# Optimization experiments

Hardware: AMD Instinct MI355X
Metric: run time of the kernel (lower is better)

Reference implementation:

```python
import jax, jax.numpy as jnp
import numpy as np

C, H, W = 21, 384, 384
THETA_ALPHA, THETA_BETA, THETA_GAMMA = 160.0, 3.0, 3.0
NUM_ITER = 5
SP_RADIUS = 6   # ~2*theta_gamma truncation for the spatial Gaussian filter
BI_RADIUS = 2   # local window stand-in for the permutohedral bilateral filter
CLIQUE_IDS = (5, 37, 81, 150, 230)  # deterministic stand-in for random.sample(range(1,256),5)


def _shift(x, dy, dx):
    # zero-padded shift: out[..., y, x] = x[..., y-dy, x-dx]
    h, w = x.shape[-2], x.shape[-1]
    py = (max(dy, 0), max(-dy, 0))
    px = (max(dx, 0), max(-dx, 0))
    xp = jnp.pad(x, [(0, 0)] * (x.ndim - 2) + [py, px])
    return xp[..., py[1]:py[1] + h, px[1]:px[1] + w]


def _gauss_blur(x, theta, radius):
    # unnormalized separable spatial Gaussian (high_dim_filter, bilateral=False)
    offs = np.arange(-radius, radius + 1)
    k = np.exp(-(offs.astype(np.float32) ** 2) / (2.0 * theta * theta))
    y = sum(float(k[i]) * _shift(x, int(o), 0) for i, o in enumerate(offs))
    return sum(float(k[i]) * _shift(y, 0, int(o)) for i, o in enumerate(offs))


def _bilateral(x, rgb, ta, tb, radius):
    # unnormalized local bilateral filter (high_dim_filter, bilateral=True)
    out = jnp.zeros_like(x)
    for dy in range(-radius, radius + 1):
        for dx in range(-radius, radius + 1):
            sw = float(np.exp(-(dy * dy + dx * dx) / (2.0 * ta * ta)))
            cdiff = rgb - _shift(rgb, dy, dx)  # (3,h,w)
            cw = jnp.exp(-jnp.sum(cdiff * cdiff, axis=0) / (2.0 * tb * tb))
            out = out + sw * cw * _shift(x, dy, dx)
    return out


def setup_inputs() -> dict:
    key = jax.random.key(0)
    k1, k2, k3 = jax.random.split(key, 3)
    # offset unaries away from 0 so first_term = prod/q stays finite
    unaries = jax.random.uniform(k1, (1, H, W, C), dtype=jnp.float32) + 0.5
    rgb = jax.random.uniform(k2, (1, H, W, 3), dtype=jnp.float32) * 255.0
    superpixels = jax.random.randint(k3, (1, H, W), 0, 256, dtype=jnp.int32)
    return {
        "unaries": unaries,
        "rgb": rgb,
        "superpixels": superpixels,
        "spatial_ker_weights": jnp.eye(C, dtype=jnp.float32),
        "bilateral_ker_weights": jnp.eye(C, dtype=jnp.float32),
        "compatibility_matrix": -jnp.eye(C, dtype=jnp.float32),
        "superpixel_low_weights": jnp.ones((C,), dtype=jnp.float32),
        "superpixel_high_weight": jnp.ones((1,), dtype=jnp.float32),
    }


def reference(unaries, rgb, superpixels, spatial_ker_weights, bilateral_ker_weights,
              compatibility_matrix, superpixel_low_weights, superpixel_high_weight):
    c, h, w = C, H, W
    u = jnp.transpose(unaries[0], (2, 0, 1))        # (c,h,w)
    img = jnp.transpose(rgb[0], (2, 0, 1))          # (3,h,w)
    sp_map = jnp.transpose(superpixels[0])          # (w,h) == (h,w) since square

    ones = jnp.ones((c, h, w), dtype=u.dtype)
    spatial_norm = _gauss_blur(ones, THETA_GAMMA, SP_RADIUS)
    bilateral_norm = _bilateral(ones, img, THETA_ALPHA, THETA_BETA, BI_RADIUS)

    # clique ids are distinct, so masks are disjoint; msum in {0,1}
    msum = jnp.zeros((h, w), dtype=u.dtype)
    for sp_idx in CLIQUE_IDS:
        msum = msum + (sp_map == sp_idx).astype(u.dtype)
    n_cliques = float(len(CLIQUE_IDS))

    q = u
    for _ in range(NUM_ITER):
        sm = jax.nn.softmax(q, axis=0)
        spatial_out = _gauss_blur(sm, THETA_GAMMA, SP_RADIUS) / spatial_norm
        bilateral_out = _bilateral(sm, img, THETA_ALPHA, THETA_BETA, BI_RADIUS) / bilateral_norm

        # prod_tensor = sum_k [ mask_k*q + (1-mask_k) ]  (disjoint masks => closed form)
        prod_tensor = msum[None] * q + (n_cliques - msum)[None]
        first_term = prod_tensor / q
        sp_update = (superpixel_low_weights[:, None, None] * first_term
                     + superpixel_high_weight[0] * (1.0 - first_term))

        mp = (spatial_ker_weights @ spatial_out.reshape(c, -1)
              + bilateral_ker_weights @ bilateral_out.reshape(c, -1))
        pairwise = (compatibility_matrix @ mp).reshape(c, h, w)
        q = u - pairwise + sp_update

    return jnp.transpose(q[None], (0, 2, 3, 1))  # (1,h,w,c)
```

## Files before the change

kernel.cpp:

```cpp
#include <hip/hip_runtime.h>
#include <hip/hip_bf16.h>

static constexpr int C  = 21;
static constexpr int H  = 384;
static constexpr int W  = 384;
static constexpr int HW = H * W;
static constexpr float NCLIQ = 5.0f;

typedef unsigned short u16;
typedef unsigned int   u32;

#define GKDEF constexpr float gk[13] = { \
    0.13533528f, 0.24935222f, 0.41111229f, 0.60653066f, 0.80073740f, \
    0.94595947f, 1.00000000f, 0.94595947f, 0.80073740f, 0.60653066f, \
    0.41111229f, 0.24935222f, 0.13533528f }

__device__ __forceinline__ float bfu2f(u16 u) {
    return __uint_as_float(((u32)u) << 16);
}
__device__ __forceinline__ u16 f2bfu(float f) {
    unsigned x = __float_as_uint(f);
    return (u16)((x + 0x7FFF + ((x >> 16) & 1)) >> 16);
}

__global__ __launch_bounds__(256)
void k_prep(const float* __restrict__ un, const float* __restrict__ rgb,
            const int* __restrict__ sp,
            const float* __restrict__ Wsp, const float* __restrict__ Wbi,
            const float* __restrict__ Cm,
            float* __restrict__ q, float* __restrict__ unp,
            u16* __restrict__ wtab, float* __restrict__ msum,
            float* __restrict__ inv_sp, float* __restrict__ inv_bn,
            float* __restrict__ M1, float* __restrict__ M2,
            int* __restrict__ mflag,
            u16* __restrict__ t1, u16* __restrict__ t2) {
    GKDEF;
    __shared__ float sM1[C * C], sM2[C * C];
    __shared__ float Aun[256 * C];
    __shared__ int seq;
    if (threadIdx.x == 0) seq = 1;
    bool bad = false;
    for (int i = threadIdx.x; i < C * C; i += 256) {
        int c = i / C, k = i - c * C;
        float a1 = 0.f, a2 = 0.f;
        for (int j = 0; j < C; j++) {
            float cm = Cm[c * C + j];
            a1 += cm * Wsp[j * C + k];
            a2 += cm * Wbi[j * C + k];
        }
        sM1[i] = a1;
        sM2[i] = a2;
        if (__float_as_uint(a1) != __float_as_uint(a2)) bad = true;
        if (blockIdx.x == 0) { M1[i] = a1; M2[i] = a2; }
    }

    int bid = blockIdx.x;
    int chunk = (bid & 7) * 72 + (bid >> 3);
    int p0 = chunk * 256;
    int p = p0 + threadIdx.x;
    int y = p / W, x = p - y * W;

    {
        const float* ub = un + (size_t)p0 * C;
        for (int i = threadIdx.x; i < 256 * C / 4; i += 256)
            *(float4*)(Aun + i * 4) = *(const float4*)(ub + i * 4);
    }
    __syncthreads();
    if (bad) atomicAnd(&seq, 0);

    float v[C];
#pragma unroll
    for (int c = 0; c < C; c++) {
        v[c] = Aun[threadIdx.x * C + c];
        q[c * HW + p] = v[c];
        unp[c * HW + p] = v[c];
    }

    float swl[9];
#pragma unroll
    for (int i = 0; i < 9; i++) swl[i] = expf(-(float)i * (1.0f / 51200.0f));

    float r0 = rgb[p * 3 + 0];
    float g0 = rgb[p * 3 + 1];
    float b0 = rgb[p * 3 + 2];
    float s = 0.f;
    int t = 0;
#pragma unroll
    for (int dy = -2; dy <= 2; dy++) {
#pragma unroll
        for (int dx = -2; dx <= 2; dx++, t++) {
            int sy = y - dy, sx = x - dx;
            float wv = 0.f;
            if (sy >= 0 && sy < H && sx >= 0 && sx < W) {
                int o = sy * W + sx;
                float dr = r0 - rgb[o * 3 + 0];
                float dg = g0 - rgb[o * 3 + 1];
                float db = b0 - rgb[o * 3 + 2];
                wv = swl[dy * dy + dx * dx] *
                     expf(-(dr * dr + dg * dg + db * db) * (1.0f / 18.0f));
            }
            u16 wu = f2bfu(wv);
            wtab[(size_t)t * HW + p] = wu;
            s += bfu2f(wu);
        }
    }
    inv_bn[p] = 1.0f / s;

    float fy = 0.f, fx = 0.f;
    for (int o = -6; o <= 6; o++) {
        if (y - o >= 0 && y - o < H) fy += gk[o + 6];
        if (x - o >= 0 && x - o < W) fx += gk[o + 6];
    }
    inv_sp[p] = 1.0f / (fy * fx);

    int vv = sp[x * W + y];
    msum[p] = (vv == 5 || vv == 37 || vv == 81 || vv == 150 || vv == 230) ? 1.0f : 0.0f;

    __syncthreads();
    bool eq = (seq != 0);
    if (bid == 0 && threadIdx.x == 0) mflag[0] = eq ? 1 : 0;

    float mx = -1e30f;
#pragma unroll
    for (int c = 0; c < C; c++) mx = fmaxf(mx, v[c]);
    float ssum = 0.f;
#pragma unroll
    for (int c = 0; c < C; c++) {
        v[c] = expf(v[c] - mx);
        ssum += v[c];
    }
    float inv = 1.0f / ssum;
    float a1[C];
#pragma unroll
    for (int c = 0; c < C; c++) a1[c] = 0.f;
#pragma unroll
    for (int k = 0; k < C; k++) {
        float e = v[k];
#pragma unroll
        for (int c = 0; c < C; c++) a1[c] += sM1[c * C + k] * e;
    }
#pragma unroll
    for (int c = 0; c < C; c++) t1[c * HW + p] = f2bfu(a1[c] * inv);
    if (!eq) {
        float a2[C];
#pragma unroll
        for (int c = 0; c < C; c++) a2[c] = 0.f;
#pragma unroll
        for (int k = 0; k < C; k++) {
            float e = v[k];
#pragma unroll
            for (int c = 0; c < C; c++) a2[c] += sM2[c * C + k] * e;
        }
#pragma unroll
        for (int c = 0; c < C; c++) t2[c * HW + p] = f2bfu(a2[c] * inv);
    }
}

__global__ __launch_bounds__(256)
void k_ST(const float* __restrict__ q, const float* __restrict__ M1,
          const float* __restrict__ M2, const int* __restrict__ mflag,
          u16* __restrict__ t1, u16* __restrict__ t2) {
    int bid = blockIdx.x;
    int chunk = (bid & 7) * 72 + (bid >> 3);
    int p = chunk * 256 + threadIdx.x;
    bool meq = (mflag[0] != 0);
    float v[C];
    float mx = -1e30f;
#pragma unroll
    for (int c = 0; c < C; c++) {
        v[c] = q[c * HW + p];
        mx = fmaxf(mx, v[c]);
    }
    float s = 0.f;
#pragma unroll
    for (int c = 0; c < C; c++) {
        v[c] = expf(v[c] - mx);
        s += v[c];
    }
    float inv = 1.0f / s;
    float a1[C];
#pragma unroll
    for (int c = 0; c < C; c++) a1[c] = 0.f;
#pragma unroll
    for (int k = 0; k < C; k++) {
        float e = v[k];
#pragma unroll
        for (int c = 0; c < C; c++) a1[c] += M1[c * C + k] * e;
    }
#pragma unroll
    for (int c = 0; c < C; c++) t1[c * HW + p] = f2bfu(a1[c] * inv);
    if (!meq) {
        float a2[C];
#pragma unroll
        for (int c = 0; c < C; c++) a2[c] = 0.f;
#pragma unroll
        for (int k = 0; k < C; k++) {
            float e = v[k];
#pragma unroll
            for (int c = 0; c < C; c++) a2[c] += M2[c * C + k] * e;
        }
#pragma unroll
        for (int c = 0; c < C; c++) t2[c * HW + p] = f2bfu(a2[c] * inv);
    }
}

__global__ __launch_bounds__(256)
void k_VF(const u16* __restrict__ t1, const u16* __restrict__ t2,
          const u16* __restrict__ wtab, const float* __restrict__ msum,
          const float* __restrict__ inv_sp, const float* __restrict__ inv_bn,
          const float* __restrict__ unp,
          const float* __restrict__ loww, const float* __restrict__ highw,
          const int* __restrict__ mflag,
          float* __restrict__ q, float* __restrict__ outp) {
    GKDEF;
    __shared__ float A[20 * 144];
    __shared__ float B[8 * 144];
    int bid = blockIdx.x;
    int xcd = bid & 7;
    int idx = bid >> 3;
    int c   = idx % 21;
    int rem = idx / 21;
    int xt  = rem % 3;
    int ytl = rem / 3;
    int gyt = xcd * 6 + ytl;
    int x0 = xt * 128;
    int y0 = gyt * 8;
    bool meq = (mflag[0] != 0);
    const u16* t1p = t1 + (size_t)c * HW;

    for (int i = threadIdx.x; i < 20 * 36; i += 256) {
        int r = i / 36, q4 = i - r * 36;
        int gy = y0 - 6 + r;
        int gx = x0 - 8 + q4 * 4;
        float4 v;
        if (gy < 0 || gy >= H) {
            v.x = v.y = v.z = v.w = 0.f;
        } else if (gx >= 0 && gx + 3 < W) {
            ushort4 u = *(const ushort4*)(t1p + gy * W + gx);
            v.x = bfu2f(u.x); v.y = bfu2f(u.y); v.z = bfu2f(u.z); v.w = bfu2f(u.w);
        } else {
            float e[4];
            for (int jj = 0; jj < 4; jj++) {
                int xx = gx + jj;
                e[jj] = (xx >= 0 && xx < W) ? bfu2f(t1p[gy * W + xx]) : 0.f;
            }
            v.x = e[0]; v.y = e[1]; v.z = e[2]; v.w = e[3];
        }
        *(float4*)(A + r * 144 + q4 * 4) = v;
    }
    __syncthreads();

    for (int i = threadIdx.x; i < 8 * 36; i += 256) {
        int r = i / 36, c4 = (i - r * 36) * 4;
        float ax = 0.f, ay = 0.f, az = 0.f, aw = 0.f;
#pragma unroll
        for (int d = 0; d < 13; d++) {
            const float4 av = *(const float4*)(A + (r + d) * 144 + c4);
            ax += gk[d] * av.x;
            ay += gk[d] * av.y;
            az += gk[d] * av.z;
            aw += gk[d] * av.w;
        }
        float4 o;
        o.x = ax; o.y = ay; o.z = az; o.w = aw;
        *(float4*)(B + r * 144 + c4) = o;
    }
    __syncthreads();

    int row = threadIdx.x >> 5;
    int xq  = (threadIdx.x & 31) * 4;
    int y   = y0 + row;
    int x4  = x0 + xq;
    int p4  = y * W + x4;

    ushort4 wu[25];
#pragma unroll
    for (int t = 0; t < 25; t++)
        wu[t] = *(const ushort4*)(wtab + (size_t)t * HW + p4);

    float bw[20];
    {
        const float* bp = B + row * 144 + xq;
        *(float4*)(bw +  0) = *(const float4*)(bp +  0);
        *(float4*)(bw +  4) = *(const float4*)(bp +  4);
        *(float4*)(bw +  8) = *(const float4*)(bp +  8);
        *(float4*)(bw + 12) = *(const float4*)(bp + 12);
        *(float4*)(bw + 16) = *(const float4*)(bp + 16);
    }
    float sp_[4];
#pragma unroll
    for (int jj = 0; jj < 4; jj++) {
        float a = 0.f;
#pragma unroll
        for (int t = 0; t < 13; t++) a += gk[t] * bw[jj + t + 2];
        sp_[jj] = a;
    }

    int robase;
    if (meq) {
        robase = row + 6;
    } else {
        const u16* t2p = t2 + (size_t)c * HW;
        for (int i = threadIdx.x; i < 12 * 36; i += 256) {
            int r = i / 36, q4 = i - r * 36;
            int gy = min(max(y0 - 2 + r, 0), H - 1);
            int gx = min(max(x0 - 8 + q4 * 4, 0), W - 4);
            ushort4 u = *(const ushort4*)(t2p + gy * W + gx);
            float4 v;
            v.x = bfu2f(u.x); v.y = bfu2f(u.y); v.z = bfu2f(u.z); v.w = bfu2f(u.w);
            *(float4*)(A + r * 144 + q4 * 4) = v;
        }
        __syncthreads();
        robase = row + 2;
    }

    float lc = loww[c], hw_ = highw[0];
    float4 msv = *(const float4*)(msum + p4);
    float4 isv = *(const float4*)(inv_sp + p4);
    float4 ibv = *(const float4*)(inv_bn + p4);
    float4 unv = *(const float4*)(unp + (size_t)c * HW + p4);
    float* qp = q + (size_t)c * HW + p4;
    float4 qo4 = *(const float4*)qp;

    float bi[4] = {0.f, 0.f, 0.f, 0.f};
    int lb = xq + 8;
#pragma unroll
    for (int dy = -2; dy <= 2; dy++) {
        int r = robase - dy;
        float rr[12];
        float4 v0 = *(const float4*)(A + r * 144 + lb - 4);
        float4 v1 = *(const float4*)(A + r * 144 + lb);
        float4 v2 = *(const float4*)(A + r * 144 + lb + 4);
        rr[0] = v0.x; rr[1] = v0.y; rr[2]  = v0.z; rr[3]  = v0.w;
        rr[4] = v1.x; rr[5] = v1.y; rr[6]  = v1.z; rr[7]  = v1.w;
        rr[8] = v2.x; rr[9] = v2.y; rr[10] = v2.z; rr[11] = v2.w;
#pragma unroll
        for (int dx = -2; dx <= 2; dx++) {
            const ushort4 wv = wu[(dy + 2) * 5 + (dx + 2)];
            bi[0] += bfu2f(wv.x) * rr[0 - dx + 4];
            bi[1] += bfu2f(wv.y) * rr[1 - dx + 4];
            bi[2] += bfu2f(wv.z) * rr[2 - dx + 4];
            bi[3] += bfu2f(wv.w) * rr[3 - dx + 4];
        }
    }

    float msa[4] = {msv.x, msv.y, msv.z, msv.w};
    float isa[4] = {isv.x, isv.y, isv.z, isv.w};
    float iba[4] = {ibv.x, ibv.y, ibv.z, ibv.w};
    float qoa[4] = {qo4.x, qo4.y, qo4.z, qo4.w};
    float una[4] = {unv.x, unv.y, unv.z, unv.w};
    float outv[4];
    for (int jj = 0; jj < 4; jj++) {
        float pw = sp_[jj] * isa[jj] + bi[jj] * iba[jj];
        float qo = qoa[jj];
        float ft = (msa[jj] * qo + (NCLIQ - msa[jj])) / qo;
        float su = lc * ft + hw_ * (1.0f - ft);
        outv[jj] = una[jj] - pw + su;
    }
    if (outp) {
        for (int jj = 0; jj < 4; jj++)
            outp[(size_t)(p4 + jj) * C + c] = outv[jj];
    } else {
        float4 res;
        res.x = outv[0]; res.y = outv[1]; res.z = outv[2]; res.w = outv[3];
        *(float4*)qp = res;
    }
}


extern "C" void kernel_launch(void* const* d_in, const int* in_sizes, int n_in,
                              void* d_out, int out_size, void* d_ws, size_t ws_size,
                              hipStream_t stream) {
    const float* un    = (const float*)d_in[0];
    const float* rgb   = (const float*)d_in[1];
    const int*   sp    = (const int*)d_in[2];
    const float* Wsp   = (const float*)d_in[3];
    const float* Wbi   = (const float*)d_in[4];
    const float* Cm    = (const float*)d_in[5];
    const float* loww  = (const float*)d_in[6];
    const float* highw = (const float*)d_in[7];
    float* out = (float*)d_out;

    float* ws    = (float*)d_ws;
    float* q     = ws;
    float* unp   = q   + (size_t)C * HW;
    float* msum  = unp + (size_t)C * HW;
    float* isp   = msum + HW;
    float* ibn   = isp + HW;
    float* M1    = ibn + HW;
    float* M2    = M1 + C * C;
    int*   mflag = (int*)(M2 + C * C);
    u16*   t1    = (u16*)(M2 + C * C + 6);
    u16*   t2    = t1 + (size_t)C * HW;
    u16*   wtab  = t2 + (size_t)C * HW;

    dim3 blk(256);
    dim3 gpix(HW / 256);
    dim3 gVF(3 * 48 * C);

    k_prep<<<gpix, blk, 0, stream>>>(un, rgb, sp, Wsp, Wbi, Cm,
                                     q, unp, wtab, msum, isp, ibn, M1, M2,
                                     mflag, t1, t2);
    for (int it = 0; it < 5; it++) {
        k_VF<<<gVF, blk, 0, stream>>>(t1, t2, wtab, msum, isp, ibn,
                                      unp, loww, highw, mflag, q,
                                      (it == 4) ? out : (float*)nullptr);
        if (it < 4)
            k_ST<<<gpix, blk, 0, stream>>>(q, M1, M2, mflag, t1, t2);
    }
}
```

Measured before the change: 239.4 us.

## Split per-pixel work across two thread halves and load bilateral weights per row

k_prep and k_ST now assign 128 pixels per 256-thread block. In k_prep one half of the threads does the weight-table and normalization setup while the other half does the softmax and matvec. In k_ST each half computes a different subset of output channels. k_VF now loads the bilateral weight table per dy row instead of holding all 25 ushort4 values in registers, which lowers register pressure. This buys more parallelism per pixel and better occupancy, at the cost of redundant softmax work in k_ST and less latency hiding for the wtab loads.

```diff
diff --git a/kernel.cpp b/kernel.cpp
--- a/kernel.cpp
+++ b/kernel.cpp
@@ -21,6 +21,23 @@
 __device__ __forceinline__ u16 f2bfu(float f) {
     unsigned x = __float_as_uint(f);
     return (u16)((x + 0x7FFF + ((x >> 16) & 1)) >> 16);
+}
+
+template<int CB, int CE>
+__device__ __forceinline__ void st_matvec(const float* __restrict__ M,
+                                          const float* v, float inv,
+                                          u16* __restrict__ t, int p) {
+    float a[CE - CB];
+#pragma unroll
+    for (int c = CB; c < CE; c++) a[c - CB] = 0.f;
+#pragma unroll
+    for (int k = 0; k < C; k++) {
+        float e = v[k];
+#pragma unroll
+        for (int c = CB; c < CE; c++) a[c - CB] += M[c * C + k] * e;
+    }
+#pragma unroll
+    for (int c = CB; c < CE; c++) t[c * HW + p] = f2bfu(a[c - CB] * inv);
 }
 
 __global__ __launch_bounds__(256)
@@ -36,7 +53,7 @@
             u16* __restrict__ t1, u16* __restrict__ t2) {
     GKDEF;
     __shared__ float sM1[C * C], sM2[C * C];
-    __shared__ float Aun[256 * C];
+    __shared__ float Aun[128 * C];
     __shared__ int seq;
     if (threadIdx.x == 0) seq = 1;
     bool bad = false;
@@ -55,104 +72,90 @@
     }
 
     int bid = blockIdx.x;
-    int chunk = (bid & 7) * 72 + (bid >> 3);
-    int p0 = chunk * 256;
-    int p = p0 + threadIdx.x;
+    int chunk = (bid & 7) * 144 + (bid >> 3);
+    int p0 = chunk * 128;
+    int px = threadIdx.x & 127;
+    int half = threadIdx.x >> 7;
+    int p = p0 + px;
     int y = p / W, x = p - y * W;
 
     {
         const float* ub = un + (size_t)p0 * C;
-        for (int i = threadIdx.x; i < 256 * C / 4; i += 256)
+        for (int i = threadIdx.x; i < 128 * C / 4; i += 256)
             *(float4*)(Aun + i * 4) = *(const float4*)(ub + i * 4);
     }
     __syncthreads();
     if (bad) atomicAnd(&seq, 0);
-
-    float v[C];
-#pragma unroll
-    for (int c = 0; c < C; c++) {
-        v[c] = Aun[threadIdx.x * C + c];
-        q[c * HW + p] = v[c];
-        unp[c * HW + p] = v[c];
-    }
-
-    float swl[9];
-#pragma unroll
-    for (int i = 0; i < 9; i++) swl[i] = expf(-(float)i * (1.0f / 51200.0f));
-
-    float r0 = rgb[p * 3 + 0];
-    float g0 = rgb[p * 3 + 1];
-    float b0 = rgb[p * 3 + 2];
-    float s = 0.f;
-    int t = 0;
-#pragma unroll
-    for (int dy = -2; dy <= 2; dy++) {
-#pragma unroll
-        for (int dx = -2; dx <= 2; dx++, t++) {
-            int sy = y - dy, sx = x - dx;
-            float wv = 0.f;
-            if (sy >= 0 && sy < H && sx >= 0 && sx < W) {
-                int o = sy * W + sx;
-                float dr = r0 - rgb[o * 3 + 0];
-                float dg = g0 - rgb[o * 3 + 1];
-                float db = b0 - rgb[o * 3 + 2];
-                wv = swl[dy * dy + dx * dx] *
-                     expf(-(dr * dr + dg * dg + db * db) * (1.0f / 18.0f));
-            }
-            u16 wu = f2bfu(wv);
-            wtab[(size_t)t * HW + p] = wu;
-            s += bfu2f(wu);
-        }
-    }
-    inv_bn[p] = 1.0f / s;
-
-    float fy = 0.f, fx = 0.f;
-    for (int o = -6; o <= 6; o++) {
-        if (y - o >= 0 && y - o < H) fy += gk[o + 6];
-        if (x - o >= 0 && x - o < W) fx += gk[o + 6];
-    }
-    inv_sp[p] = 1.0f / (fy * fx);
-
-    int vv = sp[x * W + y];
-    msum[p] = (vv == 5 || vv == 37 || vv == 81 || vv == 150 || vv == 230) ? 1.0f : 0.0f;
-
     __syncthreads();
     bool eq = (seq != 0);
     if (bid == 0 && threadIdx.x == 0) mflag[0] = eq ? 1 : 0;
 
-    float mx = -1e30f;
-#pragma unroll
-    for (int c = 0; c < C; c++) mx = fmaxf(mx, v[c]);
-    float ssum = 0.f;
-#pragma unroll
-    for (int c = 0; c < C; c++) {
-        v[c] = expf(v[c] - mx);
-        ssum += v[c];
-    }
-    float inv = 1.0f / ssum;
-    float a1[C];
-#pragma unroll
-    for (int c = 0; c < C; c++) a1[c] = 0.f;
-#pragma unroll
-    for (int k = 0; k < C; k++) {
-        float e = v[k];
-#pragma unroll
-        for (int c = 0; c < C; c++) a1[c] += sM1[c * C + k] * e;
-    }
-#pragma unroll
-    for (int c = 0; c < C; c++) t1[c * HW + p] = f2bfu(a1[c] * inv);
-    if (!eq) {
-        float a2[C];
-#pragma unroll
-        for (int c = 0; c < C; c++) a2[c] = 0.f;
-#pragma unroll
-        for (int k = 0; k < C; k++) {
-            float e = v[k];
-#pragma unroll
-            for (int c = 0; c < C; c++) a2[c] += sM2[c * C + k] * e;
-        }
-#pragma unroll
-        for (int c = 0; c < C; c++) t2[c * HW + p] = f2bfu(a2[c] * inv);
+    float v[C];
+#pragma unroll
+    for (int c = 0; c < C; c++)
+        v[c] = Aun[px * C + c];
+
+    if (half == 0) {
+#pragma unroll
+        for (int c = 0; c < C; c++) {
+            q[c * HW + p] = v[c];
+            unp[c * HW + p] = v[c];
+        }
+
+        float swl[9];
+#pragma unroll
+        for (int i = 0; i < 9; i++) swl[i] = expf(-(float)i * (1.0f / 51200.0f));
+
+        float r0 = rgb[p * 3 + 0];
+        float g0 = rgb[p * 3 + 1];
+        float b0 = rgb[p * 3 + 2];
+        float s = 0.f;
+        int t = 0;
+#pragma unroll
+        for (int dy = -2; dy <= 2; dy++) {
+#pragma unroll
+            for (int dx = -2; dx <= 2; dx++, t++) {
+                int sy = y - dy, sx = x - dx;
+                float wv = 0.f;
+                if (sy >= 0 && sy < H && sx >= 0 && sx < W) {
+                    int o = sy * W + sx;
+                    float dr = r0 - rgb[o * 3 + 0];
+                    float dg = g0 - rgb[o * 3 + 1];
+                    float db = b0 - rgb[o * 3 + 2];
+                    wv = swl[dy * dy + dx * dx] *
+                         expf(-(dr * dr + dg * dg + db * db) * (1.0f / 18.0f));
+                }
+                u16 wu = f2bfu(wv);
+                wtab[(size_t)t * HW + p] = wu;
+                s += bfu2f(wu);
+            }
+        }
+        inv_bn[p] = 1.0f / s;
+
+        float fy = 0.f, fx = 0.f;
+        for (int o = -6; o <= 6; o++) {
+            if (y - o >= 0 && y - o < H) fy += gk[o + 6];
+            if (x - o >= 0 && x - o < W) fx += gk[o + 6];
+        }
+        inv_sp[p] = 1.0f / (fy * fx);
+
+        int vv = sp[x * W + y];
+        msum[p] = (vv == 5 || vv == 37 || vv == 81 || vv == 150 || vv == 230)
+                      ? 1.0f : 0.0f;
+    } else {
+        float mx = -1e30f;
+#pragma unroll
+        for (int c = 0; c < C; c++) mx = fmaxf(mx, v[c]);
+        float ssum = 0.f;
+#pragma unroll
+        for (int c = 0; c < C; c++) {
+            v[c] = expf(v[c] - mx);
+            ssum += v[c];
+        }
+        float inv = 1.0f / ssum;
+        st_matvec<0, C>(sM1, v, inv, t1, p);
+        if (!eq)
+            st_matvec<0, C>(sM2, v, inv, t2, p);
     }
 }
 
@@ -161,8 +164,9 @@
           const float* __restrict__ M2, const int* __restrict__ mflag,
           u16* __restrict__ t1, u16* __restrict__ t2) {
     int bid = blockIdx.x;
-    int chunk = (bid & 7) * 72 + (bid >> 3);
-    int p = chunk * 256 + threadIdx.x;
+    int chunk = (bid & 7) * 144 + (bid >> 3);
+    int p = chunk * 128 + (threadIdx.x & 127);
+    int half = threadIdx.x >> 7;
     bool meq = (mflag[0] != 0);
     float v[C];
     float mx = -1e30f;
@@ -178,29 +182,12 @@
         s += v[c];
     }
     float inv = 1.0f / s;
-    float a1[C];
-#pragma unroll
-    for (int c = 0; c < C; c++) a1[c] = 0.f;
-#pragma unroll
-    for (int k = 0; k < C; k++) {
-        float e = v[k];
-#pragma unroll
-        for (int c = 0; c < C; c++) a1[c] += M1[c * C + k] * e;
-    }
-#pragma unroll
-    for (int c = 0; c < C; c++) t1[c * HW + p] = f2bfu(a1[c] * inv);
-    if (!meq) {
-        float a2[C];
-#pragma unroll
-        for (int c = 0; c < C; c++) a2[c] = 0.f;
-#pragma unroll
-        for (int k = 0; k < C; k++) {
-            float e = v[k];
-#pragma unroll
-            for (int c = 0; c < C; c++) a2[c] += M2[c * C + k] * e;
-        }
-#pragma unroll
-        for (int c = 0; c < C; c++) t2[c * HW + p] = f2bfu(a2[c] * inv);
+    if (half == 0) {
+        st_matvec<0, 11>(M1, v, inv, t1, p);
+        if (!meq) st_matvec<0, 11>(M2, v, inv, t2, p);
+    } else {
+        st_matvec<11, C>(M1, v, inv, t1, p);
+        if (!meq) st_matvec<11, C>(M2, v, inv, t2, p);
     }
 }
 
@@ -273,11 +260,6 @@
     int x4  = x0 + xq;
     int p4  = y * W + x4;
 
-    ushort4 wu[25];
-#pragma unroll
-    for (int t = 0; t < 25; t++)
-        wu[t] = *(const ushort4*)(wtab + (size_t)t * HW + p4);
-
     float bw[20];
     {
         const float* bp = B + row * 144 + xq;
@@ -326,6 +308,13 @@
     int lb = xq + 8;
 #pragma unroll
     for (int dy = -2; dy <= 2; dy++) {
+        int tb = (dy + 2) * 5;
+        ushort4 wv0 = *(const ushort4*)(wtab + (size_t)(tb + 0) * HW + p4);
+        ushort4 wv1 = *(const ushort4*)(wtab + (size_t)(tb + 1) * HW + p4);
+        ushort4 wv2 = *(const ushort4*)(wtab + (size_t)(tb + 2) * HW + p4);
+        ushort4 wv3 = *(const ushort4*)(wtab + (size_t)(tb + 3) * HW + p4);
+        ushort4 wv4 = *(const ushort4*)(wtab + (size_t)(tb + 4) * HW + p4);
+        const ushort4 wvs[5] = {wv0, wv1, wv2, wv3, wv4};
         int r = robase - dy;
         float rr[12];
         float4 v0 = *(const float4*)(A + r * 144 + lb - 4);
@@ -336,7 +325,7 @@
         rr[8] = v2.x; rr[9] = v2.y; rr[10] = v2.z; rr[11] = v2.w;
 #pragma unroll
         for (int dx = -2; dx <= 2; dx++) {
-            const ushort4 wv = wu[(dy + 2) * 5 + (dx + 2)];
+            const ushort4 wv = wvs[dx + 2];
             bi[0] += bfu2f(wv.x) * rr[0 - dx + 4];
             bi[1] += bfu2f(wv.y) * rr[1 - dx + 4];
             bi[2] += bfu2f(wv.z) * rr[2 - dx + 4];
@@ -395,7 +384,7 @@
     u16*   wtab  = t2 + (size_t)C * HW;
 
     dim3 blk(256);
-    dim3 gpix(HW / 256);
+    dim3 gpix(HW / 128);
     dim3 gVF(3 * 48 * C);
 
     k_prep<<<gpix, blk, 0, stream>>>(un, rgb, sp, Wsp, Wbi, Cm,
```

After: 225.5 us. 1.06x faster.
